# Kernel tuning notes

Measured on AMD Instinct MI355X. Metric: run time of the kernel, lower is better.

The kernel has to match this reference:

```python
import jax, jax.numpy as jnp
import numpy as np

NUM_TAGS = 128
SEQ_LEN = 256
BATCH = 512
PAD_IDX = -1  # Padding.WORD_LABEL_PAD_IDX


def setup_inputs() -> dict:
    key = jax.random.key(0)
    k1, k2, k3 = jax.random.split(key, 3)
    T = NUM_TAGS
    emissions = jax.random.normal(k1, (SEQ_LEN, BATCH, T), dtype=jnp.float32)
    tags = jax.random.randint(k2, (SEQ_LEN, BATCH), 0, T, dtype=jnp.int32)
    # transitions param: uniform(-0.1, 0.1), never transition INTO start, never FROM end
    transitions = jax.random.uniform(k3, (T + 2, T + 2), minval=-0.1, maxval=0.1, dtype=jnp.float32)
    transitions = transitions.at[:, T].set(-10000.0)      # start_tag column
    transitions = transitions.at[T + 1, :].set(-10000.0)  # end_tag row
    return {"emissions": emissions, "transitions": transitions, "tags": tags}


def reference(emissions, transitions, tags):
    T = transitions.shape[0] - 2
    start_tag, end_tag = T, T + 1
    S, B = tags.shape
    mask = (tags != PAD_IDX).astype(emissions.dtype)  # (S, B)

    # ---- numerator: joint log-likelihood of gold path ----
    # per-timestep gold emission scores, (S, B)
    emit = jnp.take_along_axis(emissions, tags[:, :, None], axis=2)[..., 0]
    llh = transitions[start_tag, tags[0]]                              # start transition
    llh = llh + jnp.sum(emit[:-1] * mask[:-1], axis=0)                 # emissions for t in [0, S-1)
    llh = llh + jnp.sum(transitions[tags[:-1], tags[1:]] * mask[1:], axis=0)  # transitions
    last_idx = mask.sum(axis=0).astype(jnp.int32) - 1                  # (B,)
    last_tags = tags[last_idx, jnp.arange(B)]
    llh = llh + transitions[last_tags, end_tag]
    llh = llh + emissions[-1, jnp.arange(B), last_tags] * mask[-1]

    # ---- denominator: log partition via forward algorithm (scan over time) ----
    trans_tt = transitions[:T, :T]                                      # (T, T)
    log_prob0 = transitions[start_tag, :T][None, :] + emissions[0]      # (B, T)

    def step(log_prob, inp):
        e, m = inp  # e: (B, T), m: (B,)
        # score[b, j] = logsumexp_i(log_prob[b, i] + trans[i, j] + e[b, j])
        score = jax.nn.logsumexp(log_prob[:, :, None] + trans_tt[None, :, :] + e[:, None, :], axis=1)
        log_prob = jnp.where(m[:, None] > 0, score, log_prob)
        return log_prob, None

    log_prob, _ = jax.lax.scan(step, log_prob0, (emissions[1:], mask[1:]))
    denom = jax.nn.logsumexp(log_prob + transitions[:T, end_tag][None, :], axis=1)  # (B,)

    return jnp.mean(llh - denom)  # reduce=True
```

## Files before the change

kernel.cpp:

```cpp
#include <hip/hip_runtime.h>

#define S_LEN 256
#define B_SZ  512
#define T_TAGS 128
#define TP2   130
#define PAD_I (-1)
#define RS    4

#define FWD_BLOCKS 32
#define NQ 32
#define QLEN 8
#define NUM_SUB 4
#define NUM_BLOCKS (NQ * NUM_SUB)
#define TOT_BLOCKS (FWD_BLOCKS + NUM_BLOCKS)
#define NTHR 192

typedef __bf16 bf16x8 __attribute__((ext_vector_type(8)));
typedef float  f32x4  __attribute__((ext_vector_type(4)));

#define PI_J(c, lg, e) ((2*(c) + ((e) >> 2))*16 + (lg)*4 + ((e) & 3))

__device__ __forceinline__ void bar_lds() {
    asm volatile("s_waitcnt lgkmcnt(0)\n\ts_barrier" ::: "memory");
}

__device__ __forceinline__ void consumer_step(
    int s, const bf16x8 (&A)[8][4], bf16x8 (&Q)[4], float &M, int tgc,
    const float (&EE)[4][8][64][4], int l)
{
    f32x4 d[8];
    const f32x4 z = {0.f, 0.f, 0.f, 0.f};
    #pragma unroll
    for (int jt = 0; jt < 8; ++jt) {
        d[jt] = __builtin_amdgcn_mfma_f32_16x16x32_bf16(A[jt][0], Q[0], z, 0, 0, 0);
        #pragma unroll
        for (int c = 1; c < 4; ++c)
            d[jt] = __builtin_amdgcn_mfma_f32_16x16x32_bf16(A[jt][c], Q[c], d[jt], 0, 0, 0);
    }
    float u[8][4];
    #pragma unroll
    for (int jt = 0; jt < 8; ++jt) {
        const f32x4 ee = *(const f32x4*)&EE[s & 3][jt][l][0];
        #pragma unroll
        for (int r = 0; r < 4; ++r) u[jt][r] = d[jt][r] * ee[r];
    }
    float Mn = M;
    if ((s & (RS - 1)) == 0) {
        float R = u[0][0];
        #pragma unroll
        for (int jt = 0; jt < 8; ++jt)
            #pragma unroll
            for (int r = 0; r < 4; ++r) R = fmaxf(R, u[jt][r]);
        R = fmaxf(R, __shfl_xor(R, 16));
        R = fmaxf(R, __shfl_xor(R, 32));
        const float rr = 1.0f / R;
        Mn = M + __logf(R);
        #pragma unroll
        for (int jt = 0; jt < 8; ++jt)
            #pragma unroll
            for (int r = 0; r < 4; ++r) u[jt][r] *= rr;
    }
    bf16x8 Qn[4];
    #pragma unroll
    for (int c = 0; c < 4; ++c)
        #pragma unroll
        for (int e = 0; e < 8; ++e)
            Qn[c][e] = (__bf16)u[2*c + (e >> 2)][e & 3];
    const bool live = (tgc != PAD_I);
    M = live ? Mn : M;
    #pragma unroll
    for (int c = 0; c < 4; ++c) Q[c] = live ? Qn[c] : Q[c];
}

__global__ __launch_bounds__(NTHR) void crf_main(
    const float* __restrict__ em,
    const float* __restrict__ trans,
    const int*   __restrict__ tags,
    float* __restrict__ denom_out,
    float* __restrict__ pl,
    int*   __restrict__ pc,
    unsigned int* __restrict__ counter,
    float* __restrict__ out)
{
    __shared__ __align__(16) float EE[4][8][64][4];
    __shared__ int lastflag;
    const int t = threadIdx.x;

    if (blockIdx.x < FWD_BLOCKS) {
        const int w  = t >> 6;
        const int l  = t & 63;
        const int lm = l & 15;
        const int lg = l >> 4;
        const int b0 = blockIdx.x * 16;

        if (w == 0) {
            bf16x8 A[8][4];
            #pragma unroll
            for (int jt = 0; jt < 8; ++jt)
                #pragma unroll
                for (int c = 0; c < 4; ++c)
                    #pragma unroll
                    for (int e = 0; e < 8; ++e)
                        A[jt][c][e] = (__bf16)__expf(trans[PI_J(c, lg, e)*TP2 + jt*16 + lm]);

            f32x4 em0[8];
            #pragma unroll
            for (int jt = 0; jt < 8; ++jt)
                em0[jt] = *(const f32x4*)&em[((size_t)0*B_SZ + b0 + lm)*T_TAGS + jt*16 + lg*4];
            bf16x8 Q[4];
            #pragma unroll
            for (int c = 0; c < 4; ++c)
                #pragma unroll
                for (int e = 0; e < 8; ++e) {
                    const int j  = PI_J(c, lg, e);
                    const int jt = 2*c + (e >> 2);
                    const int r  = e & 3;
                    Q[c][e] = (__bf16)__expf(trans[T_TAGS*TP2 + j] + em0[jt][r]);
                }
            float M = 0.f;
            int tg_cur = tags[1*B_SZ + b0 + lm];
            int tg_nxt = tags[2*B_SZ + b0 + lm];
            bar_lds();

            for (int s = 1; s <= S_LEN - 2; ++s) {
                const int sf = (s + 2 < S_LEN) ? s + 2 : S_LEN - 1;
                const int tg_fut = tags[sf*B_SZ + b0 + lm];
                consumer_step(s, A, Q, M, tg_cur, EE, l);
                tg_cur = tg_nxt; tg_nxt = tg_fut;
                bar_lds();
            }
            consumer_step(S_LEN - 1, A, Q, M, tg_cur, EE, l);

            float sum = 0.f;
            #pragma unroll
            for (int c = 0; c < 4; ++c)
                #pragma unroll
                for (int e = 0; e < 8; ++e)
                    sum += (float)Q[c][e] * __expf(trans[PI_J(c, lg, e)*TP2 + (T_TAGS + 1)]);
            sum += __shfl_xor(sum, 16);
            sum += __shfl_xor(sum, 32);
            if (l < 16)
                denom_out[b0 + l] = M + __logf(sum);
        } else {
            const int pj = (w - 1) * 4;
            auto LOADV = [&](f32x4 (&dst)[4], int s) {
                #pragma unroll
                for (int q = 0; q < 4; ++q)
                    dst[q] = *(const f32x4*)&em[((size_t)s*B_SZ + b0 + lm)*T_TAGS + (pj + q)*16 + lg*4];
            };
            auto EXPW = [&](int slot, const f32x4 (&src)[4]) {
                #pragma unroll
                for (int q = 0; q < 4; ++q) {
                    f32x4 v;
                    #pragma unroll
                    for (int r = 0; r < 4; ++r) v[r] = __expf(src[q][r]);
                    *(f32x4*)&EE[slot][pj + q][l][0] = v;
                }
            };
            f32x4 t0[4], t1[4], sA[4], sB[4];
            LOADV(t0, 1); LOADV(t1, 2);
            EXPW(1, t0);  EXPW(2, t1);
            LOADV(sB, 3); LOADV(sA, 4);
            bar_lds();

            for (int i = 1; i <= 253; i += 2) {
                EXPW((i + 2) & 3, sB);
                { const int s4 = (i + 4 < S_LEN) ? i + 4 : S_LEN - 1; LOADV(sB, s4); }
                bar_lds();
                EXPW((i + 3) & 3, sA);
                { const int s5 = (i + 5 < S_LEN) ? i + 5 : S_LEN - 1; LOADV(sA, s5); }
                bar_lds();
            }
        }
    } else {
        if (t < 128) {
            const int nb = blockIdx.x - FWD_BLOCKS;
            const int q  = nb >> 2;
            const int b  = (nb & 3) * 128 + t;
            const int s0 = q * QLEN;

            int tg[QLEN + 1];
            tg[0] = (s0 == 0) ? PAD_I : tags[(s0 - 1)*B_SZ + b];
            #pragma unroll
            for (int k = 0; k < QLEN; ++k)
                tg[k + 1] = tags[(s0 + k)*B_SZ + b];

            float acc = 0.f;
            int cnt = 0;
            if (q == 0) {
                const int t0  = tg[1];
                const int t0w = (t0 < 0) ? t0 + TP2 : t0;
                acc += trans[T_TAGS*TP2 + t0w];
            }
            #pragma unroll
            for (int k = 0; k < QLEN; ++k) {
                const int s = s0 + k;
                const int c = tg[k + 1];
                const float m = (c != PAD_I) ? 1.f : 0.f;
                cnt += (c != PAD_I) ? 1 : 0;
                if (s >= 1) {
                    const int p  = tg[k];
                    const int pw = (p < 0) ? p + TP2 : p;
                    const int cw = (c < 0) ? c + TP2 : c;
                    acc += trans[pw*TP2 + cw] * m;
                }
                if (s <= S_LEN - 2) {
                    int cc = c; if (cc < 0) cc = 0;
                    acc += em[((size_t)s*B_SZ + b)*T_TAGS + cc] * m;
                }
            }
            pl[q*B_SZ + b] = acc;
            pc[q*B_SZ + b] = cnt;
        }
    }

    __threadfence();
    if (t == 0) {
        const unsigned old = atomicAdd(counter, 1u);
        lastflag = (old == TOT_BLOCKS - 1) ? 1 : 0;
    }
    __syncthreads();
    if (lastflag) {
        __threadfence();
        float part = 0.f;
        for (int b = t; b < B_SZ; b += NTHR) {
            float llh = 0.f;
            int cnt = 0;
            #pragma unroll
            for (int q = 0; q < NQ; ++q) {
                llh += pl[q*B_SZ + b];
                cnt += pc[q*B_SZ + b];
            }
            int li = cnt - 1; if (li < 0) li = 0;
            const int lt  = tags[li*B_SZ + b];
            const int ltw = (lt < 0) ? lt + TP2 : lt;
            llh += trans[ltw*TP2 + (T_TAGS + 1)];
            const float ml = (tags[(S_LEN - 1)*B_SZ + b] != PAD_I) ? 1.f : 0.f;
            int ltc = lt; if (ltc < 0) ltc = 0;
            llh += em[((size_t)(S_LEN - 1)*B_SZ + b)*T_TAGS + ltc] * ml;
            part += llh - denom_out[b];
        }
        #pragma unroll
        for (int off = 32; off; off >>= 1)
            part += __shfl_xor(part, off);
        float* red = &EE[0][0][0][0];
        if ((t & 63) == 0) red[t >> 6] = part;
        __syncthreads();
        if (t == 0)
            out[0] = (red[0] + red[1] + red[2]) * (1.f / (float)B_SZ);
    }
}

extern "C" void kernel_launch(void* const* d_in, const int* in_sizes, int n_in,
                              void* d_out, int out_size, void* d_ws, size_t ws_size,
                              hipStream_t stream) {
    const float* em    = (const float*)d_in[0];
    const float* trans = (const float*)d_in[1];
    const int*   tags  = (const int*)d_in[2];
    float* out   = (float*)d_out;

    float* denom = (float*)d_ws;
    float* pl    = denom + B_SZ;
    int*   pc    = (int*)(pl + NQ*B_SZ);
    unsigned int* counter = (unsigned int*)(pc + NQ*B_SZ);

    hipMemsetAsync(counter, 0, sizeof(unsigned int), stream);
    crf_main<<<TOT_BLOCKS, NTHR, 0, stream>>>(em, trans, tags, denom, pl, pc, counter, out);
}
```

Before: 248.4 us.

## Fold emission exp prefetch into single-wave forward loop, drop LDS producer waves

Removes the two producer waves that computed exp(emissions) into LDS and the per-step barriers, so the single MFMA wave now loads emissions three steps ahead into registers and exponentiates them itself, interleaved with the MFMAs. The loop is unrolled by four, with templated phase indices so the rescale check becomes compile-time. Blocks shrink to one wave, and the gold-path blocks double in count to keep coverage. This cuts the barrier-synchronization latency on the serial recurrence but raises register pressure and puts the exp and load work on the critical wave.

```diff
diff --git a/kernel.cpp b/kernel.cpp
--- a/kernel.cpp
+++ b/kernel.cpp
@@ -5,29 +5,35 @@
 #define T_TAGS 128
 #define TP2   130
 #define PAD_I (-1)
-#define RS    4
 
 #define FWD_BLOCKS 32
 #define NQ 32
 #define QLEN 8
-#define NUM_SUB 4
-#define NUM_BLOCKS (NQ * NUM_SUB)
+#define NSUB 8
+#define NUM_BLOCKS (NQ * NSUB)
 #define TOT_BLOCKS (FWD_BLOCKS + NUM_BLOCKS)
-#define NTHR 192
+#define NTHR 64
 
 typedef __bf16 bf16x8 __attribute__((ext_vector_type(8)));
 typedef float  f32x4  __attribute__((ext_vector_type(4)));
 
 #define PI_J(c, lg, e) ((2*(c) + ((e) >> 2))*16 + (lg)*4 + ((e) & 3))
 
-__device__ __forceinline__ void bar_lds() {
-    asm volatile("s_waitcnt lgkmcnt(0)\n\ts_barrier" ::: "memory");
-}
-
-__device__ __forceinline__ void consumer_step(
-    int s, const bf16x8 (&A)[8][4], bf16x8 (&Q)[4], float &M, int tgc,
-    const float (&EE)[4][8][64][4], int l)
+template<int PH>
+__device__ __forceinline__ void fwd_step(
+    int s, const float* __restrict__ em, const int* __restrict__ tags,
+    int b0, int lm, int lg,
+    const bf16x8 (&A)[8][4], bf16x8 (&Q)[4], float &M,
+    f32x4 (&raw)[4][8], f32x4 (&ee)[2][8],
+    int &tgA, int &tgB, int &tgC)
 {
+    const int sl = (s + 3 < S_LEN) ? (s + 3) : (S_LEN - 1);
+    const float* ldp = &em[((size_t)sl * B_SZ + b0 + lm) * T_TAGS + lg * 4];
+    #pragma unroll
+    for (int q = 0; q < 8; ++q)
+        raw[(PH + 3) & 3][q] = *(const f32x4*)&ldp[q * 16];
+    const int tgD = tags[sl * B_SZ + b0 + lm];
+
     f32x4 d[8];
     const f32x4 z = {0.f, 0.f, 0.f, 0.f};
     #pragma unroll
@@ -37,15 +43,26 @@
         for (int c = 1; c < 4; ++c)
             d[jt] = __builtin_amdgcn_mfma_f32_16x16x32_bf16(A[jt][c], Q[c], d[jt], 0, 0, 0);
     }
+
+    #pragma unroll
+    for (int q = 0; q < 8; ++q) {
+        const f32x4 v = raw[(PH + 1) & 3][q];
+        f32x4 w;
+        #pragma unroll
+        for (int r = 0; r < 4; ++r) w[r] = __expf(v[r]);
+        ee[(PH + 1) & 1][q] = w;
+    }
+
     float u[8][4];
     #pragma unroll
     for (int jt = 0; jt < 8; ++jt) {
-        const f32x4 ee = *(const f32x4*)&EE[s & 3][jt][l][0];
-        #pragma unroll
-        for (int r = 0; r < 4; ++r) u[jt][r] = d[jt][r] * ee[r];
-    }
+        const f32x4 e4 = ee[PH & 1][jt];
+        #pragma unroll
+        for (int r = 0; r < 4; ++r) u[jt][r] = d[jt][r] * e4[r];
+    }
+
     float Mn = M;
-    if ((s & (RS - 1)) == 0) {
+    if (PH == 0) {
         float R = u[0][0];
         #pragma unroll
         for (int jt = 0; jt < 8; ++jt)
@@ -60,19 +77,22 @@
             #pragma unroll
             for (int r = 0; r < 4; ++r) u[jt][r] *= rr;
     }
+
     bf16x8 Qn[4];
     #pragma unroll
     for (int c = 0; c < 4; ++c)
         #pragma unroll
         for (int e = 0; e < 8; ++e)
             Qn[c][e] = (__bf16)u[2*c + (e >> 2)][e & 3];
-    const bool live = (tgc != PAD_I);
+    const bool live = (tgA != PAD_I);
     M = live ? Mn : M;
     #pragma unroll
     for (int c = 0; c < 4; ++c) Q[c] = live ? Qn[c] : Q[c];
+
+    tgA = tgB; tgB = tgC; tgC = tgD;
 }
 
-__global__ __launch_bounds__(NTHR) void crf_main(
+__global__ __launch_bounds__(NTHR, 1) void crf_main(
     const float* __restrict__ em,
     const float* __restrict__ trans,
     const int*   __restrict__ tags,
@@ -82,148 +102,129 @@
     unsigned int* __restrict__ counter,
     float* __restrict__ out)
 {
-    __shared__ __align__(16) float EE[4][8][64][4];
-    __shared__ int lastflag;
     const int t = threadIdx.x;
 
     if (blockIdx.x < FWD_BLOCKS) {
-        const int w  = t >> 6;
-        const int l  = t & 63;
-        const int lm = l & 15;
-        const int lg = l >> 4;
+        const int lm = t & 15;
+        const int lg = t >> 4;
         const int b0 = blockIdx.x * 16;
 
-        if (w == 0) {
-            bf16x8 A[8][4];
-            #pragma unroll
-            for (int jt = 0; jt < 8; ++jt)
-                #pragma unroll
-                for (int c = 0; c < 4; ++c)
-                    #pragma unroll
-                    for (int e = 0; e < 8; ++e)
-                        A[jt][c][e] = (__bf16)__expf(trans[PI_J(c, lg, e)*TP2 + jt*16 + lm]);
-
-            f32x4 em0[8];
-            #pragma unroll
-            for (int jt = 0; jt < 8; ++jt)
-                em0[jt] = *(const f32x4*)&em[((size_t)0*B_SZ + b0 + lm)*T_TAGS + jt*16 + lg*4];
-            bf16x8 Q[4];
-            #pragma unroll
-            for (int c = 0; c < 4; ++c)
-                #pragma unroll
-                for (int e = 0; e < 8; ++e) {
-                    const int j  = PI_J(c, lg, e);
-                    const int jt = 2*c + (e >> 2);
-                    const int r  = e & 3;
-                    Q[c][e] = (__bf16)__expf(trans[T_TAGS*TP2 + j] + em0[jt][r]);
-                }
-            float M = 0.f;
-            int tg_cur = tags[1*B_SZ + b0 + lm];
-            int tg_nxt = tags[2*B_SZ + b0 + lm];
-            bar_lds();
-
-            for (int s = 1; s <= S_LEN - 2; ++s) {
-                const int sf = (s + 2 < S_LEN) ? s + 2 : S_LEN - 1;
-                const int tg_fut = tags[sf*B_SZ + b0 + lm];
-                consumer_step(s, A, Q, M, tg_cur, EE, l);
-                tg_cur = tg_nxt; tg_nxt = tg_fut;
-                bar_lds();
-            }
-            consumer_step(S_LEN - 1, A, Q, M, tg_cur, EE, l);
-
-            float sum = 0.f;
+        bf16x8 A[8][4];
+        #pragma unroll
+        for (int jt = 0; jt < 8; ++jt)
             #pragma unroll
             for (int c = 0; c < 4; ++c)
                 #pragma unroll
                 for (int e = 0; e < 8; ++e)
-                    sum += (float)Q[c][e] * __expf(trans[PI_J(c, lg, e)*TP2 + (T_TAGS + 1)]);
-            sum += __shfl_xor(sum, 16);
-            sum += __shfl_xor(sum, 32);
-            if (l < 16)
-                denom_out[b0 + l] = M + __logf(sum);
-        } else {
-            const int pj = (w - 1) * 4;
-            auto LOADV = [&](f32x4 (&dst)[4], int s) {
-                #pragma unroll
-                for (int q = 0; q < 4; ++q)
-                    dst[q] = *(const f32x4*)&em[((size_t)s*B_SZ + b0 + lm)*T_TAGS + (pj + q)*16 + lg*4];
-            };
-            auto EXPW = [&](int slot, const f32x4 (&src)[4]) {
-                #pragma unroll
-                for (int q = 0; q < 4; ++q) {
-                    f32x4 v;
-                    #pragma unroll
-                    for (int r = 0; r < 4; ++r) v[r] = __expf(src[q][r]);
-                    *(f32x4*)&EE[slot][pj + q][l][0] = v;
-                }
-            };
-            f32x4 t0[4], t1[4], sA[4], sB[4];
-            LOADV(t0, 1); LOADV(t1, 2);
-            EXPW(1, t0);  EXPW(2, t1);
-            LOADV(sB, 3); LOADV(sA, 4);
-            bar_lds();
-
-            for (int i = 1; i <= 253; i += 2) {
-                EXPW((i + 2) & 3, sB);
-                { const int s4 = (i + 4 < S_LEN) ? i + 4 : S_LEN - 1; LOADV(sB, s4); }
-                bar_lds();
-                EXPW((i + 3) & 3, sA);
-                { const int s5 = (i + 5 < S_LEN) ? i + 5 : S_LEN - 1; LOADV(sA, s5); }
-                bar_lds();
-            }
-        }
+                    A[jt][c][e] = (__bf16)__expf(trans[PI_J(c, lg, e)*TP2 + jt*16 + lm]);
+
+        f32x4 em0[8];
+        #pragma unroll
+        for (int jt = 0; jt < 8; ++jt)
+            em0[jt] = *(const f32x4*)&em[((size_t)0*B_SZ + b0 + lm)*T_TAGS + jt*16 + lg*4];
+        bf16x8 Q[4];
+        #pragma unroll
+        for (int c = 0; c < 4; ++c)
+            #pragma unroll
+            for (int e = 0; e < 8; ++e) {
+                const int j  = PI_J(c, lg, e);
+                const int jt = 2*c + (e >> 2);
+                const int r  = e & 3;
+                Q[c][e] = (__bf16)__expf(trans[T_TAGS*TP2 + j] + em0[jt][r]);
+            }
+        float M = 0.f;
+
+        f32x4 raw[4][8];
+        f32x4 ee[2][8];
+        #pragma unroll
+        for (int sp = 1; sp <= 3; ++sp) {
+            const float* ldp = &em[((size_t)sp*B_SZ + b0 + lm)*T_TAGS + lg*4];
+            #pragma unroll
+            for (int q = 0; q < 8; ++q)
+                raw[sp][q] = *(const f32x4*)&ldp[q * 16];
+        }
+        #pragma unroll
+        for (int q = 0; q < 8; ++q) {
+            f32x4 w;
+            #pragma unroll
+            for (int r = 0; r < 4; ++r) w[r] = __expf(raw[1][q][r]);
+            ee[1][q] = w;
+        }
+        int tgA = tags[1*B_SZ + b0 + lm];
+        int tgB = tags[2*B_SZ + b0 + lm];
+        int tgC = tags[3*B_SZ + b0 + lm];
+
+        for (int s = 1; s <= S_LEN - 7; s += 4) {
+            fwd_step<1>(s,     em, tags, b0, lm, lg, A, Q, M, raw, ee, tgA, tgB, tgC);
+            fwd_step<2>(s + 1, em, tags, b0, lm, lg, A, Q, M, raw, ee, tgA, tgB, tgC);
+            fwd_step<3>(s + 2, em, tags, b0, lm, lg, A, Q, M, raw, ee, tgA, tgB, tgC);
+            fwd_step<0>(s + 3, em, tags, b0, lm, lg, A, Q, M, raw, ee, tgA, tgB, tgC);
+        }
+        fwd_step<1>(S_LEN - 3, em, tags, b0, lm, lg, A, Q, M, raw, ee, tgA, tgB, tgC);
+        fwd_step<2>(S_LEN - 2, em, tags, b0, lm, lg, A, Q, M, raw, ee, tgA, tgB, tgC);
+        fwd_step<3>(S_LEN - 1, em, tags, b0, lm, lg, A, Q, M, raw, ee, tgA, tgB, tgC);
+
+        float sum = 0.f;
+        #pragma unroll
+        for (int c = 0; c < 4; ++c)
+            #pragma unroll
+            for (int e = 0; e < 8; ++e)
+                sum += (float)Q[c][e] * __expf(trans[PI_J(c, lg, e)*TP2 + (T_TAGS + 1)]);
+        sum += __shfl_xor(sum, 16);
+        sum += __shfl_xor(sum, 32);
+        if (t < 16)
+            denom_out[b0 + t] = M + __logf(sum);
     } else {
-        if (t < 128) {
-            const int nb = blockIdx.x - FWD_BLOCKS;
-            const int q  = nb >> 2;
-            const int b  = (nb & 3) * 128 + t;
-            const int s0 = q * QLEN;
-
-            int tg[QLEN + 1];
-            tg[0] = (s0 == 0) ? PAD_I : tags[(s0 - 1)*B_SZ + b];
-            #pragma unroll
-            for (int k = 0; k < QLEN; ++k)
-                tg[k + 1] = tags[(s0 + k)*B_SZ + b];
-
-            float acc = 0.f;
-            int cnt = 0;
-            if (q == 0) {
-                const int t0  = tg[1];
-                const int t0w = (t0 < 0) ? t0 + TP2 : t0;
-                acc += trans[T_TAGS*TP2 + t0w];
-            }
-            #pragma unroll
-            for (int k = 0; k < QLEN; ++k) {
-                const int s = s0 + k;
-                const int c = tg[k + 1];
-                const float m = (c != PAD_I) ? 1.f : 0.f;
-                cnt += (c != PAD_I) ? 1 : 0;
-                if (s >= 1) {
-                    const int p  = tg[k];
-                    const int pw = (p < 0) ? p + TP2 : p;
-                    const int cw = (c < 0) ? c + TP2 : c;
-                    acc += trans[pw*TP2 + cw] * m;
-                }
-                if (s <= S_LEN - 2) {
-                    int cc = c; if (cc < 0) cc = 0;
-                    acc += em[((size_t)s*B_SZ + b)*T_TAGS + cc] * m;
-                }
-            }
-            pl[q*B_SZ + b] = acc;
-            pc[q*B_SZ + b] = cnt;
-        }
+        const int nb = blockIdx.x - FWD_BLOCKS;
+        const int q  = nb >> 3;
+        const int b  = (nb & 7) * NTHR + t;
+        const int s0 = q * QLEN;
+
+        int tg[QLEN + 1];
+        tg[0] = (s0 == 0) ? PAD_I : tags[(s0 - 1)*B_SZ + b];
+        #pragma unroll
+        for (int k = 0; k < QLEN; ++k)
+            tg[k + 1] = tags[(s0 + k)*B_SZ + b];
+
+        float acc = 0.f;
+        int cnt = 0;
+        if (q == 0) {
+            const int t0  = tg[1];
+            const int t0w = (t0 < 0) ? t0 + TP2 : t0;
+            acc += trans[T_TAGS*TP2 + t0w];
+        }
+        #pragma unroll
+        for (int k = 0; k < QLEN; ++k) {
+            const int s = s0 + k;
+            const int c = tg[k + 1];
+            const float m = (c != PAD_I) ? 1.f : 0.f;
+            cnt += (c != PAD_I) ? 1 : 0;
+            if (s >= 1) {
+                const int p  = tg[k];
+                const int pw = (p < 0) ? p + TP2 : p;
+                const int cw = (c < 0) ? c + TP2 : c;
+                acc += trans[pw*TP2 + cw] * m;
+            }
+            if (s <= S_LEN - 2) {
+                int cc = c; if (cc < 0) cc = 0;
+                acc += em[((size_t)s*B_SZ + b)*T_TAGS + cc] * m;
+            }
+        }
+        pl[q*B_SZ + b] = acc;
+        pc[q*B_SZ + b] = cnt;
     }
 
     __threadfence();
-    if (t == 0) {
-        const unsigned old = atomicAdd(counter, 1u);
-        lastflag = (old == TOT_BLOCKS - 1) ? 1 : 0;
-    }
-    __syncthreads();
-    if (lastflag) {
+    int lf = 0;
+    if (t == 0)
+        lf = (atomicAdd(counter, 1u) == TOT_BLOCKS - 1) ? 1 : 0;
+    lf = __shfl(lf, 0);
+    if (lf) {
         __threadfence();
         float part = 0.f;
-        for (int b = t; b < B_SZ; b += NTHR) {
+        #pragma unroll
+        for (int bb = 0; bb < B_SZ / NTHR; ++bb) {
+            const int b = bb * NTHR + t;
             float llh = 0.f;
             int cnt = 0;
             #pragma unroll
@@ -243,11 +244,8 @@
         #pragma unroll
         for (int off = 32; off; off >>= 1)
             part += __shfl_xor(part, off);
-        float* red = &EE[0][0][0][0];
-        if ((t & 63) == 0) red[t >> 6] = part;
-        __syncthreads();
         if (t == 0)
-            out[0] = (red[0] + red[1] + red[2]) * (1.f / (float)B_SZ);
+            out[0] = part * (1.f / (float)B_SZ);
     }
 }
 
```

New measurement: 272.2 us. 1.1x slower.
